# Kernel tuning notes

Measured on AMD Instinct MI355X. Metric: run time of the kernel, lower is better.

The kernel has to match this reference:

```python
import jax, jax.numpy as jnp
import numpy as np

N_NODES = 8192
N_GRAPHS = 16
KNN_K = 80
N_FEAT = 6
KNN_COLS = (0, 1, 2, 3)
HID = 128
HID6 = 6 * HID
N_LABELS = 3
BN_EPS = 1e-5


def knn_edges(pos, batch, k):
    # pos: [N, 4]; batch: [N] graph ids. Returns (src, tgt) with k neighbors per node,
    # restricted to same graph, excluding self (PyG knn_graph, flow source_to_target).
    n = pos.shape[0]
    sq = jnp.sum(pos * pos, axis=1)
    d2 = sq[:, None] + sq[None, :] - 2.0 * (pos @ pos.T)  # [N, N]
    valid = (batch[:, None] == batch[None, :]) & ~jnp.eye(n, dtype=bool)
    d2 = jnp.where(valid, d2, jnp.inf)
    _, idx = jax.lax.top_k(-d2, k)  # k smallest distances per row
    src = idx.reshape(-1)                      # neighbor j (message source)
    tgt = jnp.repeat(jnp.arange(n), k)         # center node i (message target)
    return src, tgt


def tag_conv(x, src, tgt, norm, W, b):
    # TAGConv K=2: out = sum_k (A_hat^k x) W_k + b, A_hat = D^-1/2 A D^-1/2
    n = x.shape[0]
    out = x @ W[0]
    h = x
    for k in range(1, W.shape[0]):
        h = jax.ops.segment_sum(norm[:, None] * h[src], tgt, num_segments=n)
        out = out + h @ W[k]
    return out + b


def pool_mean_max(x, batch, n_graphs):
    cnt = jax.ops.segment_sum(jnp.ones((x.shape[0],), x.dtype), batch, num_segments=n_graphs)
    mean = jax.ops.segment_sum(x, batch, num_segments=n_graphs) / cnt[:, None]
    mx = jax.ops.segment_max(x, batch, num_segments=n_graphs)
    return jnp.concatenate([mean, mx], axis=1)


def setup_inputs() -> dict:
    key = jax.random.key(0)
    ks = jax.random.split(key, 16)
    x = jax.random.normal(ks[0], (N_NODES, N_FEAT), dtype=jnp.float32)
    batch = jnp.repeat(jnp.arange(N_GRAPHS, dtype=jnp.int32), N_NODES // N_GRAPHS)
    s1 = 1.0 / np.sqrt(N_FEAT)
    s2 = 1.0 / np.sqrt(HID)
    s3 = 1.0 / np.sqrt(HID6)
    return {
        "x": x,
        "batch": batch,
        "conv1_w": jax.random.uniform(ks[1], (3, N_FEAT, HID), jnp.float32, -s1, s1),
        "conv1_b": jnp.zeros((HID,), jnp.float32),
        "conv2_w": jax.random.uniform(ks[2], (3, HID, HID), jnp.float32, -s2, s2),
        "conv2_b": jnp.zeros((HID,), jnp.float32),
        "conv3_w": jax.random.uniform(ks[3], (3, HID, HID), jnp.float32, -s2, s2),
        "conv3_b": jnp.zeros((HID,), jnp.float32),
        "bn_gamma": jnp.ones((HID6,), jnp.float32),
        "bn_beta": jnp.zeros((HID6,), jnp.float32),
        "bn_mean": 0.1 * jax.random.normal(ks[4], (HID6,), jnp.float32),
        "bn_var": jax.random.uniform(ks[5], (HID6,), jnp.float32, 0.5, 1.5),
        "lin_w": jax.random.uniform(ks[6], (5, HID6, HID6), jnp.float32, -s3, s3),
        "lin_b": jax.random.uniform(ks[7], (5, HID6), jnp.float32, -s3, s3),
        "out_w": jax.random.uniform(ks[8], (HID6, N_LABELS), jnp.float32, -s3, s3),
        "out_b": jax.random.uniform(ks[9], (N_LABELS,), jnp.float32, -s3, s3),
    }


def reference(x, batch, conv1_w, conv1_b, conv2_w, conv2_b, conv3_w, conv3_b,
              bn_gamma, bn_beta, bn_mean, bn_var, lin_w, lin_b, out_w, out_b):
    n = x.shape[0]
    pos = x[:, jnp.array(KNN_COLS)]
    src, tgt = knn_edges(pos, batch, KNN_K)
    # gcn_norm without self loops (edge dropout disabled: eval-mode determinism)
    deg = jax.ops.segment_sum(jnp.ones_like(src, dtype=x.dtype), tgt, num_segments=n)
    dinv = jnp.where(deg > 0, jax.lax.rsqrt(jnp.maximum(deg, 1.0)), 0.0)
    norm = dinv[src] * dinv[tgt]

    h = jax.nn.leaky_relu(tag_conv(x, src, tgt, norm, conv1_w, conv1_b))
    p1 = pool_mean_max(h, batch, N_GRAPHS)
    h = jax.nn.leaky_relu(tag_conv(h, src, tgt, norm, conv2_w, conv2_b))
    p2 = pool_mean_max(h, batch, N_GRAPHS)
    h = jax.nn.leaky_relu(tag_conv(h, src, tgt, norm, conv3_w, conv3_b))
    p3 = pool_mean_max(h, batch, N_GRAPHS)

    g = jnp.concatenate([p1, p2, p3], axis=1)  # [B, 768]
    g = (g - bn_mean) * jax.lax.rsqrt(bn_var + BN_EPS) * bn_gamma + bn_beta
    for i in range(lin_w.shape[0]):
        g = jax.nn.leaky_relu(g @ lin_w[i] + lin_b[i])
    out = g @ out_w + out_b
    return out.reshape(-1, N_LABELS)
```

## Files before the change

kernel.cpp:

```cpp
#include <hip/hip_runtime.h>

constexpr int N    = 8192;
constexpr int NPG  = 512;
constexpr int NG   = 16;
constexpr int KNN  = 80;
constexpr int F0   = 6;
constexpr int HID  = 128;
constexpr int H6   = 768;
constexpr int RPB  = 16;
constexpr int BPGR = NPG / RPB;

__device__ __forceinline__ float leaky(float v) { return v > 0.0f ? v : 0.01f * v; }

__device__ __forceinline__ int lanes_below(unsigned long long m) {
    return __builtin_amdgcn_mbcnt_hi((unsigned)(m >> 32),
           __builtin_amdgcn_mbcnt_lo((unsigned)m, 0));
}

__device__ __forceinline__ int wave_count_sum(int c) {
    int total = 0;
    #pragma unroll
    for (int b = 0; b < 4; b++)
        total += (int)__popcll(__ballot((c >> b) & 1)) << b;
    return total;
}

__global__ __launch_bounds__(256) void knn_kernel(const float* __restrict__ x,
                                                  int* __restrict__ nbr) {
    constexpr int BPG = 128;
    const int tid  = threadIdx.x;
    const int lane = tid & 63;
    const int wv   = tid >> 6;
    const int base = (blockIdx.x / BPG) << 9;
    const int t    = base + (blockIdx.x & (BPG - 1)) * 4 + wv;
    const int tl   = t - base;

    __shared__ float px[512], py[512], pz[512], pw[512];
    __shared__ unsigned long long skey[4 * 128];

    for (int j = tid; j < 512; j += 256) {
        const float* row = x + (size_t)(base + j) * F0;
        const float2 ra = *(const float2*)(row);
        const float2 rb = *(const float2*)(row + 2);
        px[j] = ra.x; py[j] = ra.y; pz[j] = rb.x; pw[j] = rb.y;
    }
    __syncthreads();

    const float tx = px[tl], ty = py[tl], tz = pz[tl], tw = pw[tl];
    const float sqt = tx*tx + ty*ty + tz*tz + tw*tw;

    unsigned d2m[8];
    #pragma unroll
    for (int j = 0; j < 8; j++) {
        const int node = j * 64 + lane;
        const float jx = px[node], jy = py[node], jz = pz[node], jw = pw[node];
        const float sqj = jx*jx + jy*jy + jz*jz + jw*jw;
        const float dot = tx*jx + ty*jy + tz*jz + tw*jw;
        const float d2  = sqt + sqj - 2.0f * dot;
        unsigned u = __float_as_uint(d2);
        u = (u & 0x80000000u) ? ~u : (u | 0x80000000u);
        d2m[j] = (node == tl) ? 0xFFFFFFFFu : u;
    }

    unsigned V = 0;
    for (int b = 31; b >= 0; --b) {
        const unsigned test = V | (1u << b);
        int c = 0;
        #pragma unroll
        for (int j = 0; j < 8; j++) c += (d2m[j] < test) ? 1 : 0;
        if (wave_count_sum(c) < KNN) V = test;
    }

    int c = 0;
    #pragma unroll
    for (int j = 0; j < 8; j++) c += (d2m[j] < V) ? 1 : 0;
    const int n_lt = wave_count_sum(c);
    const int need = KNN - n_lt;

    const int woff = wv * 128;
    int cnt_total = 0, taken = 0;
    #pragma unroll
    for (int j = 0; j < 8; j++) {
        const bool lt = d2m[j] < V;
        const bool eq = d2m[j] == V;
        const unsigned long long meq = __ballot(eq);
        const bool sel = lt || (eq && (taken + lanes_below(meq)) < need);
        taken += (int)__popcll(meq);
        const unsigned long long msel = __ballot(sel);
        if (sel) {
            const int pos = cnt_total + lanes_below(msel);
            skey[woff + pos] = ((unsigned long long)d2m[j] << 32)
                             | (unsigned)(base + j * 64 + lane);
        }
        cnt_total += (int)__popcll(msel);
    }
    for (int i = KNN + lane; i < 128; i += 64) skey[woff + i] = ~0ULL;
    __syncthreads();

    for (int kk = 2; kk <= 128; kk <<= 1) {
        for (int jj = kk >> 1; jj >= 1; jj >>= 1) {
            const int i  = ((lane & ~(jj - 1)) << 1) | (lane & (jj - 1));
            const int ix = i | jj;
            const unsigned long long a = skey[woff + i];
            const unsigned long long b = skey[woff + ix];
            const bool up = ((i & kk) == 0);
            if ((a > b) == up) { skey[woff + i] = b; skey[woff + ix] = a; }
            __syncthreads();
        }
    }

    if (lane < KNN)      nbr[t * KNN + lane]      = (int)(unsigned)skey[woff + lane];
    if (lane + 64 < KNN) nbr[t * KNN + lane + 64] = (int)(unsigned)skey[woff + lane + 64];
}

__global__ __launch_bounds__(256) void prop6(const float* __restrict__ hin,
                                             const int* __restrict__ nbr,
                                             float* __restrict__ hout) {
    const int gid = blockIdx.x * 256 + threadIdx.x;
    const int t   = gid >> 3;
    const int sl  = gid & 7;
    const int* nb = nbr + t * KNN + sl * 10;

    float a[F0] = {0.f, 0.f, 0.f, 0.f, 0.f, 0.f};
    #pragma unroll
    for (int j = 0; j < 10; j++) {
        const float* r = hin + (size_t)nb[j] * F0;
        #pragma unroll
        for (int f = 0; f < F0; f++) a[f] += r[f];
    }
    #pragma unroll
    for (int off = 1; off < 8; off <<= 1)
        #pragma unroll
        for (int f = 0; f < F0; f++) a[f] += __shfl_xor(a[f], off);

    if (sl == 0) {
        const float inv = 1.0f / 80.0f;
        float* o = hout + (size_t)t * F0;
        #pragma unroll
        for (int f = 0; f < F0; f++) o[f] = a[f] * inv;
    }
}

__global__ __launch_bounds__(256) void prop128(const float* __restrict__ hin,
                                               const int* __restrict__ nbr,
                                               float* __restrict__ hout) {
    const int bid   = blockIdx.x;
    const int slot  = bid & 7;
    const int g     = slot + (bid >> 9) * 8;
    const int chunk = (bid >> 3) & 63;
    const int lane  = threadIdx.x & 31;
    const int t     = (g << 9) + chunk * 8 + (threadIdx.x >> 5);
    const int* nb   = nbr + t * KNN;
    float a0=0.f,a1=0.f,a2=0.f,a3=0.f;
    for (int i = 0; i < KNN; i += 16) {
        const int4 sA = *(const int4*)(nb + i);
        const int4 sB = *(const int4*)(nb + i + 4);
        const int4 sC = *(const int4*)(nb + i + 8);
        const int4 sD = *(const int4*)(nb + i + 12);
        const int idx[16] = {sA.x,sA.y,sA.z,sA.w, sB.x,sB.y,sB.z,sB.w,
                             sC.x,sC.y,sC.z,sC.w, sD.x,sD.y,sD.z,sD.w};
        float4 v[16];
        #pragma unroll
        for (int q = 0; q < 16; q++)
            v[q] = *(const float4*)(hin + (size_t)idx[q] * HID + lane * 4);
        #pragma unroll
        for (int q = 0; q < 16; q += 4) {
            a0 += (v[q].x + v[q+1].x) + (v[q+2].x + v[q+3].x);
            a1 += (v[q].y + v[q+1].y) + (v[q+2].y + v[q+3].y);
            a2 += (v[q].z + v[q+1].z) + (v[q+2].z + v[q+3].z);
            a3 += (v[q].w + v[q+1].w) + (v[q+2].w + v[q+3].w);
        }
    }
    const float inv = 1.0f / 80.0f;
    float4 r; r.x=a0*inv; r.y=a1*inv; r.z=a2*inv; r.w=a3*inv;
    *(float4*)(hout + (size_t)t * HID + lane * 4) = r;
}

template<int K>
__global__ __launch_bounds__(256) void combine_kernel(const float* __restrict__ X,
                                                      const float* __restrict__ Y1,
                                                      const float* __restrict__ Y2,
                                                      const float* __restrict__ W,
                                                      const float* __restrict__ bias,
                                                      float* __restrict__ out,
                                                      float* __restrict__ psum,
                                                      float* __restrict__ pmax) {
    __shared__ float xs[3][RPB * K];
    const int tid  = threadIdx.x;
    const int row0 = blockIdx.x * RPB;

    {
        const float* s0 = X  + (size_t)row0 * K;
        const float* s1 = Y1 + (size_t)row0 * K;
        const float* s2 = Y2 + (size_t)row0 * K;
        if constexpr ((K & 3) == 0) {
            constexpr int NV = RPB * K / 4;
            for (int i = tid; i < NV; i += 256) ((float4*)xs[0])[i] = ((const float4*)s0)[i];
            for (int i = tid; i < NV; i += 256) ((float4*)xs[1])[i] = ((const float4*)s1)[i];
            for (int i = tid; i < NV; i += 256) ((float4*)xs[2])[i] = ((const float4*)s2)[i];
        } else {
            for (int i = tid; i < RPB * K; i += 256) xs[0][i] = s0[i];
            for (int i = tid; i < RPB * K; i += 256) xs[1][i] = s1[i];
            for (int i = tid; i < RPB * K; i += 256) xs[2][i] = s2[i];
        }
    }
    __syncthreads();

    const int c  = tid & 127;
    const int r0 = (tid >> 7) * 8;

    float acc[8];
    #pragma unroll
    for (int r = 0; r < 8; r++) acc[r] = 0.0f;

    #pragma unroll
    for (int s = 0; s < 3; s++) {
        const float* __restrict__ Ws   = W + (size_t)s * K * HID;
        const float* __restrict__ xseg = xs[s] + r0 * K;
        for (int k = 0; k < K; k += 2) {
            const float w0 = Ws[(size_t)k * HID + c];
            const float w1 = Ws[(size_t)(k + 1) * HID + c];
            #pragma unroll
            for (int r = 0; r < 8; r++)
                acc[r] += xseg[r * K + k] * w0 + xseg[r * K + k + 1] * w1;
        }
    }

    const float bb = bias[c];
    float sum8 = 0.0f, mx8 = -3.402823e38f;
    #pragma unroll
    for (int r = 0; r < 8; r++) {
        const float v = leaky(acc[r] + bb);
        out[(size_t)(row0 + r0 + r) * HID + c] = v;
        sum8 += v;
        mx8 = fmaxf(mx8, v);
    }

    __shared__ float ssum[128], smx[128];
    if (r0) { ssum[c] = sum8; smx[c] = mx8; }
    __syncthreads();
    if (!r0) {
        psum[(size_t)blockIdx.x * HID + c] = sum8 + ssum[c];
        pmax[(size_t)blockIdx.x * HID + c] = fmaxf(mx8, smx[c]);
    }
}

__global__ __launch_bounds__(256) void lin0_kernel(const float* __restrict__ psum1,
                                                   const float* __restrict__ pmax1,
                                                   const float* __restrict__ psum2,
                                                   const float* __restrict__ pmax2,
                                                   const float* __restrict__ psum3,
                                                   const float* __restrict__ pmax3,
                                                   const float* __restrict__ gamma,
                                                   const float* __restrict__ beta,
                                                   const float* __restrict__ mean,
                                                   const float* __restrict__ var,
                                                   const float* __restrict__ W,
                                                   const float* __restrict__ bias,
                                                   float* __restrict__ gout) {
    const int r   = blockIdx.x / 6;
    const int cc  = blockIdx.x % 6;
    const int tid = threadIdx.x;

    __shared__ float gs[H6];
    {
        const int cv = tid >> 7;
        const int c  = tid & 127;
        const float* ps = (cv ? psum2 : psum1) + (size_t)r * BPGR * HID + c;
        const float* pm = (cv ? pmax2 : pmax1) + (size_t)r * BPGR * HID + c;
        float s = 0.0f, m = -3.402823e38f;
        #pragma unroll 8
        for (int b = 0; b < BPGR; b++) { s += ps[b * HID]; m = fmaxf(m, pm[b * HID]); }
        gs[cv * 256 + c]       = s * (1.0f / 512.0f);
        gs[cv * 256 + 128 + c] = m;
    }
    if (tid < 128) {
        const float* ps = psum3 + (size_t)r * BPGR * HID + tid;
        const float* pm = pmax3 + (size_t)r * BPGR * HID + tid;
        float s = 0.0f, m = -3.402823e38f;
        #pragma unroll 8
        for (int b = 0; b < BPGR; b++) { s += ps[b * HID]; m = fmaxf(m, pm[b * HID]); }
        gs[512 + tid]       = s * (1.0f / 512.0f);
        gs[512 + 128 + tid] = m;
    }
    __syncthreads();
    for (int k = tid; k < H6; k += 256)
        gs[k] = (gs[k] - mean[k]) * (1.0f / sqrtf(var[k] + 1e-5f)) * gamma[k] + beta[k];
    __syncthreads();

    const int c  = cc * 128 + (tid & 127);
    const int kh = tid >> 7;
    const int kb = kh * 384;
    float a0=0.f,a1=0.f,a2=0.f,a3=0.f;
    for (int k = kb; k < kb + 384; k += 4) {
        a0 += gs[k]     * W[(size_t)(k)     * H6 + c];
        a1 += gs[k + 1] * W[(size_t)(k + 1) * H6 + c];
        a2 += gs[k + 2] * W[(size_t)(k + 2) * H6 + c];
        a3 += gs[k + 3] * W[(size_t)(k + 3) * H6 + c];
    }
    __shared__ float part[256];
    part[tid] = (a0 + a1) + (a2 + a3);
    __syncthreads();
    if (kh == 0) {
        const float v = part[tid] + part[tid + 128] + bias[c];
        gout[(size_t)r * H6 + c] = leaky(v);
    }
}

__global__ __launch_bounds__(256) void lin_kernel(const float* __restrict__ gin,
                                                  const float* __restrict__ W,
                                                  const float* __restrict__ bias,
                                                  float* __restrict__ gout) {
    const int r   = blockIdx.x / 6;
    const int cc  = blockIdx.x % 6;
    const int tid = threadIdx.x;

    __shared__ float gs[H6];
    for (int k = tid; k < H6; k += 256) gs[k] = gin[(size_t)r * H6 + k];
    __syncthreads();

    const int c  = cc * 128 + (tid & 127);
    const int kh = tid >> 7;
    const int kb = kh * 384;
    float a0=0.f,a1=0.f,a2=0.f,a3=0.f;
    for (int k = kb; k < kb + 384; k += 4) {
        a0 += gs[k]     * W[(size_t)(k)     * H6 + c];
        a1 += gs[k + 1] * W[(size_t)(k + 1) * H6 + c];
        a2 += gs[k + 2] * W[(size_t)(k + 2) * H6 + c];
        a3 += gs[k + 3] * W[(size_t)(k + 3) * H6 + c];
    }
    __shared__ float part[256];
    part[tid] = (a0 + a1) + (a2 + a3);
    __syncthreads();
    if (kh == 0) {
        const float v = part[tid] + part[tid + 128] + bias[c];
        gout[(size_t)r * H6 + c] = leaky(v);
    }
}

__global__ void out_kernel(const float* __restrict__ gin,
                           const float* __restrict__ W,
                           const float* __restrict__ bias,
                           float* __restrict__ out) {
    const int tid = threadIdx.x;
    __shared__ float part[192];
    if (tid < 192) {
        const int q  = tid >> 2;
        const int r  = q / 3, c = q % 3;
        const int kq = tid & 3;
        float acc = 0.0f;
        for (int k = kq * 192; k < kq * 192 + 192; k++)
            acc += gin[(size_t)r * H6 + k] * W[(size_t)k * 3 + c];
        part[tid] = acc;
    }
    __syncthreads();
    if (tid < 48) {
        const int r = tid / 3, c = tid % 3;
        out[r * 3 + c] = part[tid*4] + part[tid*4+1] + part[tid*4+2] + part[tid*4+3] + bias[c];
    }
}

extern "C" void kernel_launch(void* const* d_in, const int* in_sizes, int n_in,
                              void* d_out, int out_size, void* d_ws, size_t ws_size,
                              hipStream_t stream) {
    const float* x        = (const float*)d_in[0];
    const float* conv1_w  = (const float*)d_in[2];
    const float* conv1_b  = (const float*)d_in[3];
    const float* conv2_w  = (const float*)d_in[4];
    const float* conv2_b  = (const float*)d_in[5];
    const float* conv3_w  = (const float*)d_in[6];
    const float* conv3_b  = (const float*)d_in[7];
    const float* bn_gamma = (const float*)d_in[8];
    const float* bn_beta  = (const float*)d_in[9];
    const float* bn_mean  = (const float*)d_in[10];
    const float* bn_var   = (const float*)d_in[11];
    const float* lin_w    = (const float*)d_in[12];
    const float* lin_b    = (const float*)d_in[13];
    const float* out_w    = (const float*)d_in[14];
    const float* out_b    = (const float*)d_in[15];

    char* ws = (char*)d_ws;
    size_t off = 0;
    auto alloc = [&](size_t bytes) {
        void* p = ws + off;
        off += (bytes + 255) & ~(size_t)255;
        return p;
    };
    int*   nbr   = (int*)  alloc((size_t)N * KNN * 4);
    float* y6a   = (float*)alloc((size_t)N * F0 * 4);
    float* y6b   = (float*)alloc((size_t)N * F0 * 4);
    float* hA    = (float*)alloc((size_t)N * HID * 4);
    float* hB    = (float*)alloc((size_t)N * HID * 4);
    float* y1    = (float*)alloc((size_t)N * HID * 4);
    float* y2    = (float*)alloc((size_t)N * HID * 4);
    float* ga    = (float*)alloc((size_t)NG * H6 * 4);
    float* gb    = (float*)alloc((size_t)NG * H6 * 4);
    float* psum1 = (float*)alloc((size_t)(N / RPB) * HID * 4);
    float* pmax1 = (float*)alloc((size_t)(N / RPB) * HID * 4);
    float* psum2 = (float*)alloc((size_t)(N / RPB) * HID * 4);
    float* pmax2 = (float*)alloc((size_t)(N / RPB) * HID * 4);
    float* psum3 = (float*)alloc((size_t)(N / RPB) * HID * 4);
    float* pmax3 = (float*)alloc((size_t)(N / RPB) * HID * 4);

    knn_kernel<<<N / 4, 256, 0, stream>>>(x, nbr);

    prop6<<<N * 8 / 256, 256, 0, stream>>>(x, nbr, y6a);
    prop6<<<N * 8 / 256, 256, 0, stream>>>(y6a, nbr, y6b);
    combine_kernel<6><<<N / RPB, 256, 0, stream>>>(x, y6a, y6b, conv1_w, conv1_b, hA, psum1, pmax1);

    prop128<<<N / 8, 256, 0, stream>>>(hA, nbr, y1);
    prop128<<<N / 8, 256, 0, stream>>>(y1, nbr, y2);
    combine_kernel<128><<<N / RPB, 256, 0, stream>>>(hA, y1, y2, conv2_w, conv2_b, hB, psum2, pmax2);

    prop128<<<N / 8, 256, 0, stream>>>(hB, nbr, y1);
    prop128<<<N / 8, 256, 0, stream>>>(y1, nbr, y2);
    combine_kernel<128><<<N / RPB, 256, 0, stream>>>(hB, y1, y2, conv3_w, conv3_b, hA, psum3, pmax3);

    lin0_kernel<<<96, 256, 0, stream>>>(psum1, pmax1, psum2, pmax2, psum3, pmax3,
                                        bn_gamma, bn_beta, bn_mean, bn_var,
                                        lin_w + 0 * H6 * H6, lin_b + 0 * H6, gb);
    lin_kernel<<<96, 256, 0, stream>>>(gb, lin_w + 1 * H6 * H6, lin_b + 1 * H6, ga);
    lin_kernel<<<96, 256, 0, stream>>>(ga, lin_w + 2 * H6 * H6, lin_b + 2 * H6, gb);
    lin_kernel<<<96, 256, 0, stream>>>(gb, lin_w + 3 * H6 * H6, lin_b + 3 * H6, ga);
    lin_kernel<<<96, 256, 0, stream>>>(ga, lin_w + 4 * H6 * H6, lin_b + 4 * H6, gb);
    out_kernel<<<1, 256, 0, stream>>>(gb, out_w, out_b, (float*)d_out);
}
```

Measured before the change: 259.2 us.

## Fuse second-hop neighbor aggregation into combine kernel with graph-grouped block order

Replaces the second prop128 launch in conv2 and conv3 with an in-kernel gather. The combine kernel now computes the 2-hop aggregate for its 16 rows directly into shared memory. This drops the y2 buffer write and reread and two kernel launches. Blocks are remapped so that consecutive blocks interleave across graphs, which is meant to keep each graph's Y1 rows warm in cache. The layer-1 combine is specialized into its own kernel with a fully unrolled K loop. The cost is that the gather runs inside a block that also does the matmul, so occupancy and latency hiding may change.

```diff
diff --git a/kernel.cpp b/kernel.cpp
--- a/kernel.cpp
+++ b/kernel.cpp
@@ -176,32 +176,119 @@
     *(float4*)(hout + (size_t)t * HID + lane * 4) = r;
 }
 
-template<int K>
-__global__ __launch_bounds__(256) void combine_kernel(const float* __restrict__ X,
-                                                      const float* __restrict__ Y1,
-                                                      const float* __restrict__ Y2,
-                                                      const float* __restrict__ W,
-                                                      const float* __restrict__ bias,
-                                                      float* __restrict__ out,
-                                                      float* __restrict__ psum,
-                                                      float* __restrict__ pmax) {
+__global__ __launch_bounds__(256) void combine6(const float* __restrict__ X,
+                                                const float* __restrict__ Y1,
+                                                const float* __restrict__ Y2,
+                                                const float* __restrict__ W,
+                                                const float* __restrict__ bias,
+                                                float* __restrict__ out,
+                                                float* __restrict__ psum,
+                                                float* __restrict__ pmax) {
+    constexpr int K = F0;
     __shared__ float xs[3][RPB * K];
     const int tid  = threadIdx.x;
     const int row0 = blockIdx.x * RPB;
 
+    for (int i = tid; i < RPB * K; i += 256) xs[0][i] = X [(size_t)row0 * K + i];
+    for (int i = tid; i < RPB * K; i += 256) xs[1][i] = Y1[(size_t)row0 * K + i];
+    for (int i = tid; i < RPB * K; i += 256) xs[2][i] = Y2[(size_t)row0 * K + i];
+    __syncthreads();
+
+    const int c  = tid & 127;
+    const int r0 = (tid >> 7) * 8;
+
+    float acc[8];
+    #pragma unroll
+    for (int r = 0; r < 8; r++) acc[r] = 0.0f;
+
+    #pragma unroll
+    for (int s = 0; s < 3; s++) {
+        const float* __restrict__ Ws   = W + (size_t)s * K * HID;
+        const float* __restrict__ xseg = xs[s] + r0 * K;
+        #pragma unroll
+        for (int k = 0; k < K; k++) {
+            const float w0 = Ws[(size_t)k * HID + c];
+            #pragma unroll
+            for (int r = 0; r < 8; r++)
+                acc[r] += xseg[r * K + k] * w0;
+        }
+    }
+
+    const float bb = bias[c];
+    float sum8 = 0.0f, mx8 = -3.402823e38f;
+    #pragma unroll
+    for (int r = 0; r < 8; r++) {
+        const float v = leaky(acc[r] + bb);
+        out[(size_t)(row0 + r0 + r) * HID + c] = v;
+        sum8 += v;
+        mx8 = fmaxf(mx8, v);
+    }
+
+    __shared__ float ssum[128], smx[128];
+    if (r0) { ssum[c] = sum8; smx[c] = mx8; }
+    __syncthreads();
+    if (!r0) {
+        psum[(size_t)blockIdx.x * HID + c] = sum8 + ssum[c];
+        pmax[(size_t)blockIdx.x * HID + c] = fmaxf(mx8, smx[c]);
+    }
+}
+
+__global__ __launch_bounds__(256) void combine128f(const float* __restrict__ X,
+                                                   const float* __restrict__ Y1,
+                                                   const int* __restrict__ nbr,
+                                                   const float* __restrict__ W,
+                                                   const float* __restrict__ bias,
+                                                   float* __restrict__ out,
+                                                   float* __restrict__ psum,
+                                                   float* __restrict__ pmax) {
+    constexpr int K = HID;
+    __shared__ float xs[3][RPB * K];
+    const int bid   = blockIdx.x;
+    const int slot  = bid & 7;
+    const int idx   = bid >> 3;
+    const int g     = slot + (idx >> 5) * 8;
+    const int chunk = idx & 31;
+    const int tile  = g * BPGR + chunk;
+    const int row0  = tile * RPB;
+    const int tid   = threadIdx.x;
+
     {
         const float* s0 = X  + (size_t)row0 * K;
         const float* s1 = Y1 + (size_t)row0 * K;
-        const float* s2 = Y2 + (size_t)row0 * K;
-        if constexpr ((K & 3) == 0) {
-            constexpr int NV = RPB * K / 4;
-            for (int i = tid; i < NV; i += 256) ((float4*)xs[0])[i] = ((const float4*)s0)[i];
-            for (int i = tid; i < NV; i += 256) ((float4*)xs[1])[i] = ((const float4*)s1)[i];
-            for (int i = tid; i < NV; i += 256) ((float4*)xs[2])[i] = ((const float4*)s2)[i];
-        } else {
-            for (int i = tid; i < RPB * K; i += 256) xs[0][i] = s0[i];
-            for (int i = tid; i < RPB * K; i += 256) xs[1][i] = s1[i];
-            for (int i = tid; i < RPB * K; i += 256) xs[2][i] = s2[i];
+        constexpr int NV = RPB * K / 4;
+        for (int i = tid; i < NV; i += 256) ((float4*)xs[0])[i] = ((const float4*)s0)[i];
+        for (int i = tid; i < NV; i += 256) ((float4*)xs[1])[i] = ((const float4*)s1)[i];
+    }
+    {
+        const int lane = tid & 31;
+        const int w8   = tid >> 5;
+        const float inv = 1.0f / 80.0f;
+        #pragma unroll
+        for (int rr = 0; rr < 2; rr++) {
+            const int r = w8 + rr * 8;
+            const int* nb = nbr + (size_t)(row0 + r) * KNN;
+            float a0=0.f,a1=0.f,a2=0.f,a3=0.f;
+            for (int i = 0; i < KNN; i += 16) {
+                const int4 sA = *(const int4*)(nb + i);
+                const int4 sB = *(const int4*)(nb + i + 4);
+                const int4 sC = *(const int4*)(nb + i + 8);
+                const int4 sD = *(const int4*)(nb + i + 12);
+                const int ix[16] = {sA.x,sA.y,sA.z,sA.w, sB.x,sB.y,sB.z,sB.w,
+                                    sC.x,sC.y,sC.z,sC.w, sD.x,sD.y,sD.z,sD.w};
+                float4 v[16];
+                #pragma unroll
+                for (int q = 0; q < 16; q++)
+                    v[q] = *(const float4*)(Y1 + (size_t)ix[q] * HID + lane * 4);
+                #pragma unroll
+                for (int q = 0; q < 16; q += 4) {
+                    a0 += (v[q].x + v[q+1].x) + (v[q+2].x + v[q+3].x);
+                    a1 += (v[q].y + v[q+1].y) + (v[q+2].y + v[q+3].y);
+                    a2 += (v[q].z + v[q+1].z) + (v[q+2].z + v[q+3].z);
+                    a3 += (v[q].w + v[q+1].w) + (v[q+2].w + v[q+3].w);
+                }
+            }
+            float4 o; o.x=a0*inv; o.y=a1*inv; o.z=a2*inv; o.w=a3*inv;
+            *(float4*)&xs[2][r * K + lane * 4] = o;
         }
     }
     __syncthreads();
@@ -240,8 +327,8 @@
     if (r0) { ssum[c] = sum8; smx[c] = mx8; }
     __syncthreads();
     if (!r0) {
-        psum[(size_t)blockIdx.x * HID + c] = sum8 + ssum[c];
-        pmax[(size_t)blockIdx.x * HID + c] = fmaxf(mx8, smx[c]);
+        psum[(size_t)tile * HID + c] = sum8 + ssum[c];
+        pmax[(size_t)tile * HID + c] = fmaxf(mx8, smx[c]);
     }
 }
 
@@ -392,7 +479,6 @@
     float* hA    = (float*)alloc((size_t)N * HID * 4);
     float* hB    = (float*)alloc((size_t)N * HID * 4);
     float* y1    = (float*)alloc((size_t)N * HID * 4);
-    float* y2    = (float*)alloc((size_t)N * HID * 4);
     float* ga    = (float*)alloc((size_t)NG * H6 * 4);
     float* gb    = (float*)alloc((size_t)NG * H6 * 4);
     float* psum1 = (float*)alloc((size_t)(N / RPB) * HID * 4);
@@ -406,15 +492,13 @@
 
     prop6<<<N * 8 / 256, 256, 0, stream>>>(x, nbr, y6a);
     prop6<<<N * 8 / 256, 256, 0, stream>>>(y6a, nbr, y6b);
-    combine_kernel<6><<<N / RPB, 256, 0, stream>>>(x, y6a, y6b, conv1_w, conv1_b, hA, psum1, pmax1);
+    combine6<<<N / RPB, 256, 0, stream>>>(x, y6a, y6b, conv1_w, conv1_b, hA, psum1, pmax1);
 
     prop128<<<N / 8, 256, 0, stream>>>(hA, nbr, y1);
-    prop128<<<N / 8, 256, 0, stream>>>(y1, nbr, y2);
-    combine_kernel<128><<<N / RPB, 256, 0, stream>>>(hA, y1, y2, conv2_w, conv2_b, hB, psum2, pmax2);
+    combine128f<<<N / RPB, 256, 0, stream>>>(hA, y1, nbr, conv2_w, conv2_b, hB, psum2, pmax2);
 
     prop128<<<N / 8, 256, 0, stream>>>(hB, nbr, y1);
-    prop128<<<N / 8, 256, 0, stream>>>(y1, nbr, y2);
-    combine_kernel<128><<<N / RPB, 256, 0, stream>>>(hB, y1, y2, conv3_w, conv3_b, hA, psum3, pmax3);
+    combine128f<<<N / RPB, 256, 0, stream>>>(hB, y1, nbr, conv3_w, conv3_b, hA, psum3, pmax3);
 
     lin0_kernel<<<96, 256, 0, stream>>>(psum1, pmax1, psum2, pmax2, psum3, pmax3,
                                         bn_gamma, bn_beta, bn_mean, bn_var,
```

After: 249.0 us. -4.0%, faster.
